# Optimization experiments

Hardware: AMD Instinct MI355X
Metric: run time of the kernel (lower is better)

## Reference

```python
import jax, jax.numpy as jnp
import numpy as np

N = 50000      # query points
N0 = 50000     # support points
M = 32         # neighbors per query
K = 15         # kernel points
DIM = 3
D_IN = 64
D_OUT = 64
POINT_INFLUENCE = 1.0
KERNEL_RADIUS = 1.5 * POINT_INFLUENCE  # _INFLUENCE_TO_RADIUS * point_influence


def setup_inputs() -> dict:
    key = jax.random.key(0)
    k1, k2, k3, k4, k5 = jax.random.split(key, 5)
    query_points = jax.random.normal(k1, (N, DIM), jnp.float32)
    support_points = jax.random.normal(k2, (N0, DIM), jnp.float32)
    neighbors = jax.random.randint(k3, (N, M), 0, N0 + 1)  # index N0 = shadow point
    x = jax.random.normal(k4, (N0, D_IN), jnp.float32)
    # Kernel point dispositions: fixed center point, rest spread within kernel radius
    # (stand-in for kernel_point_optimization_debug; K_points is a frozen parameter).
    rng = np.random.RandomState(0)
    kp = rng.uniform(-1.0, 1.0, (K, DIM))
    kp[0, :] = 0.0
    kp = kp * (KERNEL_RADIUS / np.max(np.linalg.norm(kp, axis=1)))
    K_points = jnp.asarray(kp, dtype=jnp.float32)
    # Xavier-normal conv weights [K, D_IN, D_OUT]
    std = (2.0 / (D_IN + D_OUT)) ** 0.5
    weight = jax.random.normal(k5, (K, D_IN, D_OUT), jnp.float32) * std
    return {
        "query_points": query_points,
        "support_points": support_points,
        "neighbors": neighbors,
        "x": x,
        "K_points": K_points,
        "weight": weight,
    }


def reference(query_points, support_points, neighbors, x, K_points, weight):
    # Shadow support point far away + zero shadow feature row
    shadow = jnp.full((1, query_points.shape[1]), 1e6, dtype=support_points.dtype)
    sp = jnp.concatenate([support_points, shadow], axis=0)            # [N0+1, 3]
    xp = jnp.concatenate([x, jnp.zeros((1, x.shape[1]), x.dtype)], axis=0)  # [N0+1, d]

    # Gather neighbor coords, center on query point
    neighb_pts = sp[neighbors] - query_points[:, None, :]             # [N, M, 3]
    # Squared distances to each kernel point
    diff = neighb_pts[:, :, None, :] - K_points[None, None, :, :]     # [N, M, K, 3]
    sq_distances = jnp.sum(diff * diff, axis=-1)                      # [N, M, K]

    # Linear influence, then transpose to [N, K, M]
    all_weights = jnp.clip(1.0 - jnp.sqrt(sq_distances) / POINT_INFLUENCE, 0.0)
    all_weights = jnp.swapaxes(all_weights, 1, 2)                     # [N, K, M]

    # Gather neighbor features and aggregate per kernel point
    feats = xp[neighbors]                                             # [N, M, d]
    weighted = jnp.einsum("nkm,nmd->nkd", all_weights, feats)        # [N, K, d]
    # Apply per-kernel-point weight matrices and sum over kernel points
    out = jnp.einsum("nkd,kdo->no", weighted, weight)                # [N, out]
    return out
```

## Files before the change

### kernel.cpp

```cpp
#include <hip/hip_runtime.h>

#define NQ 50000
#define NS 50000
#define MNB 32
#define KP 15
#define DF 64
#define WTS 968
#define WQS 40

typedef __bf16 bf16x8 __attribute__((ext_vector_type(8)));
typedef float  f32x4  __attribute__((ext_vector_type(4)));

__device__ __forceinline__ unsigned short f2bf(float f) {
    union { float f; unsigned int u; } v; v.f = f;
    unsigned int u = v.u;
    return (unsigned short)((u + 0x7FFFu + ((u >> 16) & 1u)) >> 16);
}

__global__ __launch_bounds__(256) void conv_x(const float* __restrict__ x,
                                              unsigned int* __restrict__ xb, int n4) {
    const int i = blockIdx.x * 256 + threadIdx.x;
    if (i * 4 + 3 < n4) {
        const float4* s = (const float4*)x + i * 2;
        const float4 a0 = s[0], a1 = s[1];
        uint4 o;
        o.x = (unsigned)f2bf(a0.x) | ((unsigned)f2bf(a0.y) << 16);
        o.y = (unsigned)f2bf(a0.z) | ((unsigned)f2bf(a0.w) << 16);
        o.z = (unsigned)f2bf(a1.x) | ((unsigned)f2bf(a1.y) << 16);
        o.w = (unsigned)f2bf(a1.z) | ((unsigned)f2bf(a1.w) << 16);
        ((uint4*)xb)[i] = o;
    }
}

__global__ __launch_bounds__(256) void conv_w(const float* __restrict__ W,
                                              uint4* __restrict__ wBf) {
    const int chunk = blockIdx.x * 256 + threadIdx.x;
    if (chunk >= 7680) return;
    const int tc = chunk >> 6, c = chunk & 63;
    union { unsigned short s[8]; uint4 u; } pk;
    #pragma unroll
    for (int j = 0; j < 8; ++j) {
        const int kappa = tc * 8 + j;
        const int k  = kappa >> 6;
        const int cb = kappa & 3;
        const int t  = (kappa >> 2) & 15;
        pk.s[j] = f2bf(W[(size_t)(k * 64 + cb * 16 + t) * 64 + c]);
    }
    wBf[chunk] = pk.u;
}

__global__ __launch_bounds__(1024, 8) void kpconv_fused(
    const float* __restrict__ qp, const float* __restrict__ sp,
    const int* __restrict__ nb, const unsigned short* __restrict__ xbu,
    const float* __restrict__ kpts, const uint4* __restrict__ wBf,
    float* __restrict__ out)
{
    __shared__ struct {
        __align__(16) unsigned short wt[16 * WTS];
        __align__(16) unsigned short wq[16][16 * WQS];
        __align__(16) unsigned int   ids[16][MNB];
    } sm;

    const int tid  = threadIdx.x;
    const int lane = tid & 63, wv = tid >> 6;
    const int kh = lane >> 5, m = lane & 31;
    const int n0 = blockIdx.x * 16;
    const int n  = n0 + wv;

    const int id = nb[n * MNB + m];
    const float qx = qp[n * 3 + 0], qy = qp[n * 3 + 1], qz = qp[n * 3 + 2];
    float sx = 1e6f, sy = 1e6f, sz = 1e6f;
    if (id < NS) { sx = sp[id * 3 + 0]; sy = sp[id * 3 + 1]; sz = sp[id * 3 + 2]; }
    const float rx = sx - qx, ry = sy - qy, rz = sz - qz;
    float wk[8];
    #pragma unroll
    for (int j = 0; j < 8; ++j) {
        const int k = kh * 8 + j;
        const int kc = (k < KP) ? k : 0;
        const float dx = rx - kpts[kc * 3 + 0];
        const float dy = ry - kpts[kc * 3 + 1];
        const float dz = rz - kpts[kc * 3 + 2];
        wk[j] = fmaxf(1.0f - sqrtf(dx * dx + dy * dy + dz * dz), 0.0f);
    }
    #pragma unroll
    for (int j = 0; j < 8; ++j) {
        const int k = kh * 8 + j;
        if (k < KP) sm.wq[wv][k * WQS + m] = f2bf(wk[j]);
    }
    if (kh == 0) sm.ids[wv][m] = (id < NS) ? (unsigned)id : 0u;

    const int cl = lane & 15, q = lane >> 4;
    union { uint4 u; bf16x8 v; } af;
    af.u = *(const uint4*)&sm.wq[wv][cl * WQS + q * 8];
    const uint4 ia = *(const uint4*)&sm.ids[wv][q * 8];
    const uint4 ib = *(const uint4*)&sm.ids[wv][q * 8 + 4];
    const f32x4 zero = (f32x4){0.f, 0.f, 0.f, 0.f};
    f32x4 acc1[4];
    #pragma unroll
    for (int cb = 0; cb < 4; ++cb) {
        const unsigned v0 = xbu[(size_t)ia.x * DF + cb * 16 + cl];
        const unsigned v1 = xbu[(size_t)ia.y * DF + cb * 16 + cl];
        const unsigned v2 = xbu[(size_t)ia.z * DF + cb * 16 + cl];
        const unsigned v3 = xbu[(size_t)ia.w * DF + cb * 16 + cl];
        const unsigned v4 = xbu[(size_t)ib.x * DF + cb * 16 + cl];
        const unsigned v5 = xbu[(size_t)ib.y * DF + cb * 16 + cl];
        const unsigned v6 = xbu[(size_t)ib.z * DF + cb * 16 + cl];
        const unsigned v7 = xbu[(size_t)ib.w * DF + cb * 16 + cl];
        union { uint4 u; bf16x8 v; } bf;
        bf.u.x = v0 | (v1 << 16);
        bf.u.y = v2 | (v3 << 16);
        bf.u.z = v4 | (v5 << 16);
        bf.u.w = v6 | (v7 << 16);
        acc1[cb] = __builtin_amdgcn_mfma_f32_16x16x32_bf16(af.v, bf.v, zero, 0, 0, 0);
    }

    #pragma unroll
    for (int i = 0; i < 4; ++i) {
        const int k = q * 4 + i;
        if (k < KP) {
            union { unsigned short s[4]; uint2 u; } pk;
            #pragma unroll
            for (int cb = 0; cb < 4; ++cb) pk.s[cb] = f2bf(acc1[cb][i]);
            *(uint2*)&sm.wt[wv * WTS + (k * 16 + cl) * 4] = pk.u;
        }
    }
    __syncthreads();
    if (wv >= 4) return;

    f32x4 dacc = (f32x4){0.f, 0.f, 0.f, 0.f};
    #pragma unroll 6
    for (int ks = 0; ks < 30; ++ks) {
        const bf16x8 a = *(const bf16x8*)&sm.wt[cl * WTS + ks * 32 + q * 8];
        union { uint4 u; bf16x8 v; } bu;
        bu.u = wBf[(4 * ks + q) * 64 + wv * 16 + cl];
        dacc = __builtin_amdgcn_mfma_f32_16x16x32_bf16(a, bu.v, dacc, 0, 0, 0);
    }
    #pragma unroll
    for (int i = 0; i < 4; ++i)
        out[(size_t)(n0 + q * 4 + i) * 64 + wv * 16 + cl] = dacc[i];
}

extern "C" void kernel_launch(void* const* d_in, const int* in_sizes, int n_in,
                              void* d_out, int out_size, void* d_ws, size_t ws_size,
                              hipStream_t stream) {
    const float* qp   = (const float*)d_in[0];
    const float* sp   = (const float*)d_in[1];
    const int*   nb   = (const int*)d_in[2];
    const float* x    = (const float*)d_in[3];
    const float* kpts = (const float*)d_in[4];
    const float* W    = (const float*)d_in[5];
    float* out = (float*)d_out;

    uint4*          wBf = (uint4*)d_ws;
    unsigned int*   xb  = (unsigned int*)((char*)d_ws + 122880);
    unsigned short* xbu = (unsigned short*)xb;

    hipLaunchKernelGGL(conv_x, dim3(1563), dim3(256), 0, stream, x, xb, NS * DF / 2);
    hipLaunchKernelGGL(conv_w, dim3(30), dim3(256), 0, stream, W, wBf);
    hipLaunchKernelGGL(kpconv_fused, dim3(NQ / 16), dim3(1024), 0, stream,
                       qp, sp, nb, xbu, kpts, wBf, out);
}
```

Before: 136.2 us.

## Interleave bf16 feature layout for 8-byte gathers and merge prep kernels

Stores the bf16 copy of x in an interleaved layout so that each lane gathers its four channel-block values with one 8-byte load instead of four 2-byte loads. Those values are then repacked into MFMA operands with byte-permute instructions. It also merges the x and W conversion kernels into one launch and switches to the compiler's native bf16 conversion. The aim is fewer gather memory instructions and one fewer launch, at the cost of a permuted workspace layout that both kernels must agree on.

After: 129.3 us. 5.1% less time.

```diff
diff --git a/kernel.cpp b/kernel.cpp
--- a/kernel.cpp
+++ b/kernel.cpp
@@ -11,47 +11,48 @@
 typedef __bf16 bf16x8 __attribute__((ext_vector_type(8)));
 typedef float  f32x4  __attribute__((ext_vector_type(4)));
 
-__device__ __forceinline__ unsigned short f2bf(float f) {
-    union { float f; unsigned int u; } v; v.f = f;
-    unsigned int u = v.u;
-    return (unsigned short)((u + 0x7FFFu + ((u >> 16) & 1u)) >> 16);
+__device__ __forceinline__ unsigned short bf1(float f) {
+    union { __bf16 h; unsigned short s; } r; r.h = (__bf16)f; return r.s;
+}
+__device__ __forceinline__ unsigned pk2(float a, float b) {
+    union { __bf16 h[2]; unsigned u; } r;
+    r.h[0] = (__bf16)a; r.h[1] = (__bf16)b; return r.u;
 }
 
-__global__ __launch_bounds__(256) void conv_x(const float* __restrict__ x,
-                                              unsigned int* __restrict__ xb, int n4) {
-    const int i = blockIdx.x * 256 + threadIdx.x;
-    if (i * 4 + 3 < n4) {
-        const float4* s = (const float4*)x + i * 2;
-        const float4 a0 = s[0], a1 = s[1];
-        uint4 o;
-        o.x = (unsigned)f2bf(a0.x) | ((unsigned)f2bf(a0.y) << 16);
-        o.y = (unsigned)f2bf(a0.z) | ((unsigned)f2bf(a0.w) << 16);
-        o.z = (unsigned)f2bf(a1.x) | ((unsigned)f2bf(a1.y) << 16);
-        o.w = (unsigned)f2bf(a1.z) | ((unsigned)f2bf(a1.w) << 16);
-        ((uint4*)xb)[i] = o;
+__global__ __launch_bounds__(256) void preconv(
+    const float* __restrict__ x, const float* __restrict__ W,
+    unsigned short* __restrict__ xbp, uint4* __restrict__ wBf)
+{
+    const int b = blockIdx.x;
+    if (b < NS / 16) {
+        const int row = b * 16 + (threadIdx.x >> 4);
+        const int cl  = threadIdx.x & 15;
+        const float f0 = x[row * DF + 0 * 16 + cl];
+        const float f1 = x[row * DF + 1 * 16 + cl];
+        const float f2 = x[row * DF + 2 * 16 + cl];
+        const float f3 = x[row * DF + 3 * 16 + cl];
+        uint2 o; o.x = pk2(f0, f1); o.y = pk2(f2, f3);
+        *(uint2*)&xbp[row * DF + cl * 4] = o;
+    } else {
+        const int chunk = (b - NS / 16) * 256 + threadIdx.x;
+        if (chunk >= 7680) return;
+        const int tc = chunk >> 6, c = chunk & 63;
+        union { unsigned short s[8]; uint4 u; } pk;
+        #pragma unroll
+        for (int j = 0; j < 8; ++j) {
+            const int kappa = tc * 8 + j;
+            const int k  = kappa >> 6;
+            const int cb = kappa & 3;
+            const int t  = (kappa >> 2) & 15;
+            pk.s[j] = bf1(W[(size_t)(k * 64 + cb * 16 + t) * 64 + c]);
+        }
+        wBf[chunk] = pk.u;
     }
-}
-
-__global__ __launch_bounds__(256) void conv_w(const float* __restrict__ W,
-                                              uint4* __restrict__ wBf) {
-    const int chunk = blockIdx.x * 256 + threadIdx.x;
-    if (chunk >= 7680) return;
-    const int tc = chunk >> 6, c = chunk & 63;
-    union { unsigned short s[8]; uint4 u; } pk;
-    #pragma unroll
-    for (int j = 0; j < 8; ++j) {
-        const int kappa = tc * 8 + j;
-        const int k  = kappa >> 6;
-        const int cb = kappa & 3;
-        const int t  = (kappa >> 2) & 15;
-        pk.s[j] = f2bf(W[(size_t)(k * 64 + cb * 16 + t) * 64 + c]);
-    }
-    wBf[chunk] = pk.u;
 }
 
 __global__ __launch_bounds__(1024, 8) void kpconv_fused(
     const float* __restrict__ qp, const float* __restrict__ sp,
-    const int* __restrict__ nb, const unsigned short* __restrict__ xbu,
+    const int* __restrict__ nb, const uint2* __restrict__ xb2,
     const float* __restrict__ kpts, const uint4* __restrict__ wBf,
     float* __restrict__ out)
 {
@@ -72,7 +73,6 @@
     float sx = 1e6f, sy = 1e6f, sz = 1e6f;
     if (id < NS) { sx = sp[id * 3 + 0]; sy = sp[id * 3 + 1]; sz = sp[id * 3 + 2]; }
     const float rx = sx - qx, ry = sy - qy, rz = sz - qz;
-    float wk[8];
     #pragma unroll
     for (int j = 0; j < 8; ++j) {
         const int k = kh * 8 + j;
@@ -80,12 +80,8 @@
         const float dx = rx - kpts[kc * 3 + 0];
         const float dy = ry - kpts[kc * 3 + 1];
         const float dz = rz - kpts[kc * 3 + 2];
-        wk[j] = fmaxf(1.0f - sqrtf(dx * dx + dy * dy + dz * dz), 0.0f);
-    }
-    #pragma unroll
-    for (int j = 0; j < 8; ++j) {
-        const int k = kh * 8 + j;
-        if (k < KP) sm.wq[wv][k * WQS + m] = f2bf(wk[j]);
+        const float wkj = fmaxf(1.0f - sqrtf(dx * dx + dy * dy + dz * dz), 0.0f);
+        if (k < KP) sm.wq[wv][k * WQS + m] = bf1(wkj);
     }
     if (kh == 0) sm.ids[wv][m] = (id < NS) ? (unsigned)id : 0u;
 
@@ -94,34 +90,36 @@
     af.u = *(const uint4*)&sm.wq[wv][cl * WQS + q * 8];
     const uint4 ia = *(const uint4*)&sm.ids[wv][q * 8];
     const uint4 ib = *(const uint4*)&sm.ids[wv][q * 8 + 4];
+    const uint2 r0 = xb2[(size_t)ia.x * 16 + cl];
+    const uint2 r1 = xb2[(size_t)ia.y * 16 + cl];
+    const uint2 r2 = xb2[(size_t)ia.z * 16 + cl];
+    const uint2 r3 = xb2[(size_t)ia.w * 16 + cl];
+    const uint2 r4 = xb2[(size_t)ib.x * 16 + cl];
+    const uint2 r5 = xb2[(size_t)ib.y * 16 + cl];
+    const uint2 r6 = xb2[(size_t)ib.z * 16 + cl];
+    const uint2 r7 = xb2[(size_t)ib.w * 16 + cl];
+    #define PRM(hi, lo, sel) __builtin_amdgcn_perm((hi), (lo), (sel))
+    const unsigned S0 = 0x05040100u, S1 = 0x07060302u;
+    union { uint4 u; bf16x8 v; } bf[4];
+    bf[0].u = (uint4){PRM(r1.x, r0.x, S0), PRM(r3.x, r2.x, S0), PRM(r5.x, r4.x, S0), PRM(r7.x, r6.x, S0)};
+    bf[1].u = (uint4){PRM(r1.x, r0.x, S1), PRM(r3.x, r2.x, S1), PRM(r5.x, r4.x, S1), PRM(r7.x, r6.x, S1)};
+    bf[2].u = (uint4){PRM(r1.y, r0.y, S0), PRM(r3.y, r2.y, S0), PRM(r5.y, r4.y, S0), PRM(r7.y, r6.y, S0)};
+    bf[3].u = (uint4){PRM(r1.y, r0.y, S1), PRM(r3.y, r2.y, S1), PRM(r5.y, r4.y, S1), PRM(r7.y, r6.y, S1)};
+    #undef PRM
     const f32x4 zero = (f32x4){0.f, 0.f, 0.f, 0.f};
     f32x4 acc1[4];
     #pragma unroll
-    for (int cb = 0; cb < 4; ++cb) {
-        const unsigned v0 = xbu[(size_t)ia.x * DF + cb * 16 + cl];
-        const unsigned v1 = xbu[(size_t)ia.y * DF + cb * 16 + cl];
-        const unsigned v2 = xbu[(size_t)ia.z * DF + cb * 16 + cl];
-        const unsigned v3 = xbu[(size_t)ia.w * DF + cb * 16 + cl];
-        const unsigned v4 = xbu[(size_t)ib.x * DF + cb * 16 + cl];
-        const unsigned v5 = xbu[(size_t)ib.y * DF + cb * 16 + cl];
-        const unsigned v6 = xbu[(size_t)ib.z * DF + cb * 16 + cl];
-        const unsigned v7 = xbu[(size_t)ib.w * DF + cb * 16 + cl];
-        union { uint4 u; bf16x8 v; } bf;
-        bf.u.x = v0 | (v1 << 16);
-        bf.u.y = v2 | (v3 << 16);
-        bf.u.z = v4 | (v5 << 16);
-        bf.u.w = v6 | (v7 << 16);
-        acc1[cb] = __builtin_amdgcn_mfma_f32_16x16x32_bf16(af.v, bf.v, zero, 0, 0, 0);
-    }
+    for (int cb = 0; cb < 4; ++cb)
+        acc1[cb] = __builtin_amdgcn_mfma_f32_16x16x32_bf16(af.v, bf[cb].v, zero, 0, 0, 0);
 
     #pragma unroll
     for (int i = 0; i < 4; ++i) {
         const int k = q * 4 + i;
         if (k < KP) {
-            union { unsigned short s[4]; uint2 u; } pk;
-            #pragma unroll
-            for (int cb = 0; cb < 4; ++cb) pk.s[cb] = f2bf(acc1[cb][i]);
-            *(uint2*)&sm.wt[wv * WTS + (k * 16 + cl) * 4] = pk.u;
+            uint2 pkd;
+            pkd.x = pk2(acc1[0][i], acc1[1][i]);
+            pkd.y = pk2(acc1[2][i], acc1[3][i]);
+            *(uint2*)&sm.wt[wv * WTS + (k * 16 + cl) * 4] = pkd;
         }
     }
     __syncthreads();
@@ -152,11 +150,10 @@
     float* out = (float*)d_out;
 
     uint4*          wBf = (uint4*)d_ws;
-    unsigned int*   xb  = (unsigned int*)((char*)d_ws + 122880);
-    unsigned short* xbu = (unsigned short*)xb;
+    unsigned short* xbp = (unsigned short*)((char*)d_ws + 122880);
 
-    hipLaunchKernelGGL(conv_x, dim3(1563), dim3(256), 0, stream, x, xb, NS * DF / 2);
-    hipLaunchKernelGGL(conv_w, dim3(30), dim3(256), 0, stream, W, wBf);
+    hipLaunchKernelGGL(preconv, dim3(NS / 16 + 30), dim3(256), 0, stream,
+                       x, W, xbp, wBf);
     hipLaunchKernelGGL(kpconv_fused, dim3(NQ / 16), dim3(1024), 0, stream,
-                       qp, sp, nb, xbu, kpts, wBf, out);
+                       qp, sp, nb, (const uint2*)xbp, kpts, wBf, out);
 }
```
